# Optimization experiments

Measured on AMD Instinct MI355X. Metric: run time of the kernel, lower is better.

## Reference

```python
import jax, jax.numpy as jnp
import numpy as np

N_ATOMS = 5000
N_PAIRS = 160000
N_STRUCT = 16
N_SPECIES = 4
L_MAX = 2
K = 128            # k_max per l (rectangular)
N_BASIS = 8        # radial basis size
RAD_HIDDEN = 32    # radial MLP hidden
CUTOFF = 5.0
MSG_SCALE = 0.1767767   # ~1/sqrt(avg_degree)
INIT_SCALE = 0.2        # hypers['initial_scaling']


def _orthogonal(key, n):
    m = jax.random.normal(key, (n, n))
    q, r = jnp.linalg.qr(m)
    return q * jnp.sign(jnp.diag(r))[None, :]


def setup_inputs() -> dict:
    key = jax.random.key(0)
    ks = jax.random.split(key, 24)
    positions = jax.random.normal(ks[0], (N_ATOMS, 3)) * 1.5
    cells = jax.random.normal(ks[1], (N_STRUCT, 3, 3)) * 0.5
    species = jax.random.randint(ks[2], (N_ATOMS,), 0, N_SPECIES)
    cell_shifts = jax.random.randint(ks[3], (N_PAIRS, 3), 0, 3).astype(jnp.int32)
    center_indices = jax.random.randint(ks[4], (N_PAIRS,), 0, N_ATOMS)
    neighbor_indices = jax.random.randint(ks[5], (N_PAIRS,), 0, N_ATOMS)
    structure_pairs = jax.random.randint(ks[6], (N_PAIRS,), 0, N_STRUCT)
    s = lambda k, sh, f: jax.random.normal(k, sh) * f
    params = dict(
        embed=s(ks[7], (N_SPECIES, K), 1.0),
        rad_w1=s(ks[8], (N_BASIS, RAD_HIDDEN), 0.3), rad_b1=jnp.zeros((RAD_HIDDEN,)),
        rad_w2=s(ks[9], (RAD_HIDDEN, (L_MAX + 1) * K), 0.3), rad_b2=jnp.zeros(((L_MAX + 1) * K,)),
        erad_w1=s(ks[10], (N_BASIS, RAD_HIDDEN), 0.3), erad_b1=jnp.zeros((RAD_HIDDEN,)),
        erad_w2=s(ks[11], (RAD_HIDDEN, (L_MAX + 1) * K), 0.3), erad_b2=jnp.zeros(((L_MAX + 1) * K,)),
        mix_a=s(ks[12], (L_MAX + 1, K), 0.5),
        emix_a=s(ks[13], (L_MAX + 1, K), 0.5),
        head_w1=s(ks[14], (K, K), 0.1), head_b1=jnp.zeros((K,)),
        head_w2=s(ks[15], (K, K), 0.1), head_b2=jnp.zeros((K,)),
        last_w=s(ks[16], (K, 1), 0.1), last_b=jnp.zeros((1,)),
        U2=_orthogonal(ks[20], 9),  # orthogonal CG change-of-basis, U @ U.T = I
    )
    return dict(positions=positions, cells=cells, species=species,
                cell_shifts=cell_shifts, center_indices=center_indices,
                neighbor_indices=neighbor_indices, structure_pairs=structure_pairs,
                **params)


def _sph(unit):
    # real spherical harmonics up to l=2, inputs are unit vectors [P,3]
    x, y, z = unit[:, 0], unit[:, 1], unit[:, 2]
    sh0 = jnp.ones_like(x)[:, None]
    sh1 = jnp.stack([y, z, x], axis=1)
    c = jnp.sqrt(3.0)
    sh2 = jnp.stack([c * x * y, c * y * z, 0.5 * (3 * z * z - 1.0),
                     c * x * z, 0.5 * c * (x * x - y * y)], axis=1)
    return [sh0, sh1, sh2]


def _radial(d, w1, b1, w2, b2):
    # Gaussian radial basis * smooth cutoff -> MLP -> per-l K channels
    centers = jnp.linspace(0.0, CUTOFF, N_BASIS)
    rb = jnp.exp(-((d[:, None] - centers[None, :]) ** 2) / (2.0 * 0.5 ** 2))
    fcut = jnp.where(d < CUTOFF, 0.5 * (jnp.cos(jnp.pi * d / CUTOFF) + 1.0), 0.0)
    h = jax.nn.silu((rb * fcut[:, None]) @ w1 + b1)
    return (h @ w2 + b2).reshape(-1, L_MAX + 1, K)  # [P, l, K]


def _uncouple(f, l, U2):
    # coupled [N, 2l+1, K] -> uncoupled matrix [N, 3, 3, K] (padded_l = 2)
    if l == 0:
        return f[:, :, None, :]
    n, _, k = f.shape
    vec = jnp.zeros((n, 9, k), f.dtype)
    off = 1 if l == 1 else 4
    vec = vec.at[:, off:off + 2 * l + 1, :].set(f)
    unc = jnp.einsum('qp,nqk->npk', U2, vec)  # U2.T @ vec
    return unc.reshape(n, 3, 3, k)


def _couple(unc, l, U2):
    if l == 0:
        return unc[:, :, 0, :]
    n, k = unc.shape[0], unc.shape[-1]
    vec = jnp.einsum('pq,nqk->npk', U2, unc.reshape(n, 9, k))
    off = 1 if l == 1 else 4
    return vec[:, off:off + 2 * l + 1, :]


def _cg_iterate(feats, U2, mix):
    # CG tensor product iteration in the uncoupled (matrix) basis:
    # matrix product A@A is equivariant under A -> D A D^T
    out = []
    for l, f in enumerate(feats):
        A = _uncouple(f, l, U2)
        C = jnp.einsum('nimk,nmjk->nijk', A, A)
        out.append(_couple(A + C * mix[l][None, None, None, :], l, U2))
    return out


def _forward(positions, cells, embed, rad_w1, rad_b1, rad_w2, rad_b2,
             erad_w1, erad_b1, erad_w2, erad_b2, mix_a, emix_a,
             head_w1, head_b1, head_w2, head_b2, last_w, last_b, U2,
             species, cell_shifts, center_indices, neighbor_indices, structure_pairs):
    # pair vectors with PBC shifts
    shifts = cell_shifts.astype(positions.dtype) - 1.0  # -> {-1,0,1}
    vec = positions[neighbor_indices] - positions[center_indices] \
        + jnp.einsum('pi,pij->pj', shifts, cells[structure_pairs])
    d = jnp.sqrt(jnp.sum(vec * vec, axis=1) + 1e-12)
    unit = vec / d[:, None]
    sh = [s * INIT_SCALE for s in _sph(unit)]
    Rk = _radial(d, rad_w1, rad_b1, rad_w2, rad_b2)      # [P, 3, K]
    emb_n = embed[species][neighbor_indices]             # [P, K]

    # invariant message passing: sh_l x radial x neighbor embedding, scatter to centers
    feats = []
    for l in range(L_MAX + 1):
        msg = sh[l][:, :, None] * Rk[:, l, None, :] * emb_n[:, None, :]
        feats.append(jax.ops.segment_sum(msg, center_indices, num_segments=N_ATOMS) * MSG_SCALE)

    feats = _cg_iterate(feats, U2, mix_a)

    # equivariant message passing layer
    Rke = _radial(d, erad_w1, erad_b1, erad_w2, erad_b2)
    inv_n = feats[0][neighbor_indices, 0, :]             # [P, K] invariant part
    new = []
    for l in range(L_MAX + 1):
        g = feats[l][neighbor_indices]                   # [P, 2l+1, K]
        msg = sh[l][:, :, None] * Rke[:, l, None, :] * inv_n[:, None, :] \
            + Rke[:, 0, None, :] * g
        new.append(feats[l] + jax.ops.segment_sum(msg, center_indices, num_segments=N_ATOMS) * MSG_SCALE)

    feats = _cg_iterate(new, U2, emix_a)

    # scalar (l=0) MLP head + last linear layer
    h = feats[0][:, 0, :]
    h = jax.nn.silu(h @ head_w1 + head_b1)
    h = jax.nn.silu(h @ head_w2 + head_b2)
    return h @ last_w + last_b  # [N_ATOMS, 1]


def reference(positions, cells, species, cell_shifts, center_indices,
              neighbor_indices, structure_pairs, embed, rad_w1, rad_b1, rad_w2,
              rad_b2, erad_w1, erad_b1, erad_w2, erad_b2, mix_a, emix_a,
              head_w1, head_b1, head_w2, head_b2, last_w, last_b, U2):
    return _forward(positions, cells, embed, rad_w1, rad_b1, rad_w2, rad_b2,
                    erad_w1, erad_b1, erad_w2, erad_b2, mix_a, emix_a,
                    head_w1, head_b1, head_w2, head_b2, last_w, last_b, U2,
                    species, cell_shifts, center_indices, neighbor_indices,
                    structure_pairs)
```

## Files before the change

### kernel.cpp

```cpp
#include <hip/hip_runtime.h>

constexpr int   kAtoms  = 5000;
constexpr int   kPairs  = 160000;
constexpr int   KD      = 128;
constexpr int   NB      = 8;
constexpr int   RH      = 32;
constexpr float kCutoff = 5.0f;
constexpr float kPi     = 3.14159265358979323846f;
constexpr float C1 = 0.2f * 0.1767767f;
constexpr float C2 = 1.2f * 0.1767767f;
constexpr int   CHUNK = 32;

__device__ __forceinline__ float silu(float x) { return x / (1.0f + __expf(-x)); }


__global__ __launch_bounds__(256) void hist_kernel(
    const int* __restrict__ ctr, int* __restrict__ cnt)
{
    int p = blockIdx.x * 256 + threadIdx.x;
    atomicAdd(cnt + ctr[p], 1);
}

__global__ __launch_bounds__(1024) void scan_kernel(
    const int* __restrict__ cnt, int* __restrict__ off, int* __restrict__ cur)
{
    __shared__ int s_part[1024];
    const int CH = 5;
    int t = threadIdx.x;
    int base = t * CH;
    int loc[CH];
    int run = 0;
    #pragma unroll
    for (int i = 0; i < CH; i++) {
        int idx = base + i;
        int v = (idx < kAtoms) ? cnt[idx] : 0;
        loc[i] = run;
        run += v;
    }
    s_part[t] = run;
    __syncthreads();
    for (int st = 1; st < 1024; st <<= 1) {
        int v = (t >= st) ? s_part[t - st] : 0;
        __syncthreads();
        s_part[t] += v;
        __syncthreads();
    }
    int excl = (t > 0) ? s_part[t - 1] : 0;
    #pragma unroll
    for (int i = 0; i < CH; i++) {
        int idx = base + i;
        if (idx < kAtoms) { off[idx] = excl + loc[i]; cur[idx] = excl + loc[i]; }
    }
    if (t == 1023) off[kAtoms] = s_part[1023];
}

__global__ __launch_bounds__(256) void build_kernel(
    const float* __restrict__ pos, const float* __restrict__ cells,
    const int* __restrict__ species, const int* __restrict__ shifts,
    const int* __restrict__ ctr, const int* __restrict__ nbr,
    const int* __restrict__ spair,
    int* __restrict__ cur, int* __restrict__ nbrs_s, int* __restrict__ specs_s,
    float* __restrict__ rbf_s)
{
    int p = blockIdx.x * 256 + threadIdx.x;
    int ci = ctr[p], ni = nbr[p], sp = spair[p];
    float s0 = (float)shifts[p * 3 + 0] - 1.0f;
    float s1 = (float)shifts[p * 3 + 1] - 1.0f;
    float s2 = (float)shifts[p * 3 + 2] - 1.0f;
    const float* C = cells + sp * 9;
    float vx = pos[ni * 3 + 0] - pos[ci * 3 + 0] + s0 * C[0] + s1 * C[3] + s2 * C[6];
    float vy = pos[ni * 3 + 1] - pos[ci * 3 + 1] + s0 * C[1] + s1 * C[4] + s2 * C[7];
    float vz = pos[ni * 3 + 2] - pos[ci * 3 + 2] + s0 * C[2] + s1 * C[5] + s2 * C[8];
    float d = sqrtf(vx * vx + vy * vy + vz * vz + 1e-12f);
    float fcut = (d < kCutoff) ? 0.5f * (__cosf(kPi * d / kCutoff) + 1.0f) : 0.0f;

    int slot = atomicAdd(cur + ci, 1);
    nbrs_s[slot]  = ni;
    specs_s[slot] = species[ni];

    float r[NB];
    #pragma unroll
    for (int i = 0; i < NB; i++) {
        float tt = d - (kCutoff / (NB - 1)) * (float)i;
        r[i] = __expf(-2.0f * tt * tt) * fcut;
    }
    float4* dst = (float4*)(rbf_s + (size_t)slot * NB);
    dst[0] = make_float4(r[0], r[1], r[2], r[3]);
    dst[1] = make_float4(r[4], r[5], r[6], r[7]);
}

__global__ __launch_bounds__(128) void f0_kernel(
    const float* __restrict__ rbf_s, const int* __restrict__ specs_s,
    const int* __restrict__ off,
    const float* __restrict__ embed,
    const float* __restrict__ w1, const float* __restrict__ b1,
    const float* __restrict__ w2, const float* __restrict__ b2,
    const float* __restrict__ mix,
    float* __restrict__ G0)
{
    __shared__ float s_w1[NB][RH];
    __shared__ float s_b1v[RH];
    __shared__ float s_Hp[2][2][4][RH];
    __shared__ float s_H[2][4][RH];
    __shared__ float s_np[2][2][4];
    __shared__ float s_nc[2][4];

    int t = threadIdx.x;
    int w = t >> 6;
    int t64 = t & 63;
    for (int idx = t; idx < NB * RH; idx += 128)
        s_w1[idx >> 5][idx & 31] = w1[idx];
    if (t < RH) s_b1v[t] = b1[t];
    __syncthreads();

    int a = blockIdx.x * 2 + w;
    int start = off[a], m = off[a + 1] - start;

    int g = t64 >> 5, j = t64 & 31;
    float H0 = 0, H1 = 0, H2 = 0, H3 = 0;
    int   n0 = 0, n1 = 0, n2 = 0, n3 = 0;
    float b1j = s_b1v[j];
    for (int pr = g; pr < m; pr += 2) {
        const float* rb = rbf_s + (size_t)(start + pr) * NB;
        float acc = b1j;
        #pragma unroll
        for (int i = 0; i < NB; i++) acc += rb[i] * s_w1[i][j];
        float h = silu(acc);
        int s = specs_s[start + pr];
        H0 += (s == 0) ? h : 0.0f;  H1 += (s == 1) ? h : 0.0f;
        H2 += (s == 2) ? h : 0.0f;  H3 += (s == 3) ? h : 0.0f;
        n0 += (s == 0); n1 += (s == 1); n2 += (s == 2); n3 += (s == 3);
    }
    s_Hp[w][g][0][j] = H0; s_Hp[w][g][1][j] = H1;
    s_Hp[w][g][2][j] = H2; s_Hp[w][g][3][j] = H3;
    if (j == 0) {
        s_np[w][g][0] = (float)n0; s_np[w][g][1] = (float)n1;
        s_np[w][g][2] = (float)n2; s_np[w][g][3] = (float)n3;
    }
    __syncthreads();
    for (int e = t64; e < 4 * RH; e += 64) {
        int s = e >> 5, jj = e & 31;
        s_H[w][s][jj] = s_Hp[w][0][s][jj] + s_Hp[w][1][s][jj];
    }
    if (t64 < 4) s_nc[w][t64] = s_np[w][0][t64] + s_np[w][1][t64];
    __syncthreads();

    float nc0 = s_nc[w][0], nc1 = s_nc[w][1], nc2 = s_nc[w][2], nc3 = s_nc[w][3];
    #pragma unroll
    for (int half = 0; half < 2; half++) {
        int k = t64 + 64 * half;
        float e0 = embed[0 * KD + k], e1 = embed[1 * KD + k];
        float e2 = embed[2 * KD + k], e3 = embed[3 * KD + k];
        float P0 = 0, P1 = 0, P2 = 0, P3 = 0;
        #pragma unroll 2
        for (int jq = 0; jq < RH / 4; jq++) {
            float4 h0 = *(const float4*)&s_H[w][0][4 * jq];
            float4 h1 = *(const float4*)&s_H[w][1][4 * jq];
            float4 h2 = *(const float4*)&s_H[w][2][4 * jq];
            float4 h3 = *(const float4*)&s_H[w][3][4 * jq];
            float wa = w2[(4 * jq + 0) * (3 * KD) + k];
            float wb = w2[(4 * jq + 1) * (3 * KD) + k];
            float wc = w2[(4 * jq + 2) * (3 * KD) + k];
            float wd = w2[(4 * jq + 3) * (3 * KD) + k];
            P0 += h0.x * wa + h0.y * wb + h0.z * wc + h0.w * wd;
            P1 += h1.x * wa + h1.y * wb + h1.z * wc + h1.w * wd;
            P2 += h2.x * wa + h2.y * wb + h2.z * wc + h2.w * wd;
            P3 += h3.x * wa + h3.y * wb + h3.z * wc + h3.w * wd;
        }
        float F = b2[k] * (nc0 * e0 + nc1 * e1 + nc2 * e2 + nc3 * e3)
                + e0 * P0 + e1 * P1 + e2 * P2 + e3 * P3;
        float F0v = C1 * F;
        G0[(size_t)a * KD + k] = F0v + F0v * F0v * mix[k];
    }
}

__global__ __launch_bounds__(64, 2) void d0_kernel(
    const float* __restrict__ rbf_s, const int* __restrict__ nbrs_s,
    const int* __restrict__ off,
    const float* __restrict__ w1, const float* __restrict__ b1,
    const float* __restrict__ w2, const float* __restrict__ b2,
    const float* __restrict__ emix,
    const float* __restrict__ G0,
    float* __restrict__ V)
{
    __shared__ float s_w1[NB][RH];
    __shared__ float s_b1v[RH];
    __shared__ float s_h[CHUNK][RH];
    __shared__ int   s_nbr[CHUNK];

    int t = threadIdx.x;
    for (int idx = t; idx < NB * RH; idx += 64)
        s_w1[idx >> 5][idx & 31] = w1[idx];
    if (t < RH) s_b1v[t] = b1[t];
    __syncthreads();

    int a = blockIdx.x;
    int start = off[a], end = off[a + 1];
    int k0 = t, k1 = t + 64;

    float w2c0[RH], w2c1[RH];
    #pragma unroll
    for (int j = 0; j < RH; j++) {
        w2c0[j] = w2[j * (3 * KD) + k0];
        w2c1[j] = w2[j * (3 * KD) + k1];
    }
    float b2k0 = b2[k0], b2k1 = b2[k1];

    int g = t >> 5, j = t & 31;
    float b1j = s_b1v[j];

    float Dacc0 = 0.0f, Dacc1 = 0.0f;
    for (int c = start; c < end; c += CHUNK) {
        int m = min(CHUNK, end - c);
        __syncthreads();
        for (int pr = g; pr < m; pr += 2) {
            const float* rb = rbf_s + (size_t)(c + pr) * NB;
            float acc = b1j;
            #pragma unroll
            for (int i = 0; i < NB; i++) acc += rb[i] * s_w1[i][j];
            s_h[pr][j] = silu(acc);
        }
        if (t < m) s_nbr[t] = nbrs_s[c + t];
        __syncthreads();

        const float* gb = G0 + (size_t)s_nbr[0] * KD;
        float gv0_next = gb[k0];
        float gv1_next = gb[k1];
        for (int i = 0; i < m; i++) {
            float gv0 = gv0_next, gv1 = gv1_next;
            if (i + 1 < m) {
                const float* gn = G0 + (size_t)s_nbr[i + 1] * KD;
                gv0_next = gn[k0];
                gv1_next = gn[k1];
            }
            float R0 = b2k0, R1 = b2k1;
            #pragma unroll
            for (int jq = 0; jq < RH / 4; jq++) {
                float4 h4 = *(const float4*)&s_h[i][4 * jq];
                R0 += h4.x * w2c0[4 * jq + 0] + h4.y * w2c0[4 * jq + 1]
                    + h4.z * w2c0[4 * jq + 2] + h4.w * w2c0[4 * jq + 3];
                R1 += h4.x * w2c1[4 * jq + 0] + h4.y * w2c1[4 * jq + 1]
                    + h4.z * w2c1[4 * jq + 2] + h4.w * w2c1[4 * jq + 3];
            }
            Dacc0 += R0 * gv0;
            Dacc1 += R1 * gv1;
        }
    }
    float n0 = G0[(size_t)a * KD + k0] + C2 * Dacc0;
    float n1 = G0[(size_t)a * KD + k1] + C2 * Dacc1;
    V[(size_t)a * KD + k0] = n0 + n0 * n0 * emix[k0];
    V[(size_t)a * KD + k1] = n1 + n1 * n1 * emix[k1];
}

__global__ __launch_bounds__(128) void head_kernel(
    const float* __restrict__ V,
    const float* __restrict__ w1, const float* __restrict__ b1,
    const float* __restrict__ w2, const float* __restrict__ b2,
    const float* __restrict__ lw, const float* __restrict__ lb,
    float* __restrict__ out)
{
    __shared__ float s_a[8][KD];
    __shared__ float s_b[8][KD];
    int j = threadIdx.x;
    int abase = blockIdx.x * 8;

    #pragma unroll
    for (int a = 0; a < 8; a++) {
        int ga = abase + a;
        s_a[a][j] = (ga < kAtoms) ? V[(size_t)ga * KD + j] : 0.0f;
    }
    __syncthreads();

    float acc[8];
    float bj = b1[j];
    #pragma unroll
    for (int a = 0; a < 8; a++) acc[a] = bj;
    for (int kk = 0; kk < KD; kk += 4) {
        float wa = w1[(kk + 0) * KD + j], wb = w1[(kk + 1) * KD + j];
        float wc = w1[(kk + 2) * KD + j], wd = w1[(kk + 3) * KD + j];
        #pragma unroll
        for (int a = 0; a < 8; a++) {
            float4 v = *(const float4*)&s_a[a][kk];
            acc[a] += v.x * wa + v.y * wb + v.z * wc + v.w * wd;
        }
    }
    #pragma unroll
    for (int a = 0; a < 8; a++) s_b[a][j] = silu(acc[a]);
    __syncthreads();

    float b2j = b2[j];
    #pragma unroll
    for (int a = 0; a < 8; a++) acc[a] = b2j;
    for (int kk = 0; kk < KD; kk += 4) {
        float wa = w2[(kk + 0) * KD + j], wb = w2[(kk + 1) * KD + j];
        float wc = w2[(kk + 2) * KD + j], wd = w2[(kk + 3) * KD + j];
        #pragma unroll
        for (int a = 0; a < 8; a++) {
            float4 v = *(const float4*)&s_b[a][kk];
            acc[a] += v.x * wa + v.y * wb + v.z * wc + v.w * wd;
        }
    }
    float lwj = lw[j];
    __syncthreads();
    #pragma unroll
    for (int a = 0; a < 8; a++) s_a[a][j] = silu(acc[a]) * lwj;
    __syncthreads();
    for (int s = 64; s > 0; s >>= 1) {
        if (j < s) {
            #pragma unroll
            for (int a = 0; a < 8; a++) s_a[a][j] += s_a[a][j + s];
        }
        __syncthreads();
    }
    if (j < 8) {
        int ga = abase + j;
        if (ga < kAtoms) out[ga] = s_a[j][0] + lb[0];
    }
}

extern "C" void kernel_launch(void* const* d_in, const int* in_sizes, int n_in,
                              void* d_out, int out_size, void* d_ws, size_t ws_size,
                              hipStream_t stream) {
    const float* positions = (const float*)d_in[0];
    const float* cells     = (const float*)d_in[1];
    const int*   species   = (const int*)d_in[2];
    const int*   shifts    = (const int*)d_in[3];
    const int*   ctr       = (const int*)d_in[4];
    const int*   nbr       = (const int*)d_in[5];
    const int*   spair     = (const int*)d_in[6];
    const float* embed     = (const float*)d_in[7];
    const float* rad_w1    = (const float*)d_in[8];
    const float* rad_b1    = (const float*)d_in[9];
    const float* rad_w2    = (const float*)d_in[10];
    const float* rad_b2    = (const float*)d_in[11];
    const float* erad_w1   = (const float*)d_in[12];
    const float* erad_b1   = (const float*)d_in[13];
    const float* erad_w2   = (const float*)d_in[14];
    const float* erad_b2   = (const float*)d_in[15];
    const float* mix_a     = (const float*)d_in[16];
    const float* emix_a    = (const float*)d_in[17];
    const float* head_w1   = (const float*)d_in[18];
    const float* head_b1   = (const float*)d_in[19];
    const float* head_w2   = (const float*)d_in[20];
    const float* head_b2   = (const float*)d_in[21];
    const float* last_w    = (const float*)d_in[22];
    const float* last_b    = (const float*)d_in[23];

    float* rbf_s = (float*)d_ws;
    float* G0    = rbf_s + (size_t)kPairs * NB;
    float* V     = G0    + (size_t)kAtoms * KD;
    int*   cnt   = (int*)(V + (size_t)kAtoms * KD);
    int*   off   = cnt + kAtoms;
    int*   cur   = off + kAtoms + 1;
    int*   nbrs  = cur + kAtoms;
    int*   specs = nbrs + kPairs;

    hipMemsetAsync(cnt, 0, kAtoms * sizeof(int), stream);

    hist_kernel<<<kPairs / 256, 256, 0, stream>>>(ctr, cnt);
    scan_kernel<<<1, 1024, 0, stream>>>(cnt, off, cur);
    build_kernel<<<kPairs / 256, 256, 0, stream>>>(
        positions, cells, species, shifts, ctr, nbr, spair,
        cur, nbrs, specs, rbf_s);

    f0_kernel<<<kAtoms / 2, 128, 0, stream>>>(
        rbf_s, specs, off, embed, rad_w1, rad_b1, rad_w2, rad_b2,
        mix_a, G0);

    d0_kernel<<<kAtoms, 64, 0, stream>>>(
        rbf_s, nbrs, off, erad_w1, erad_b1, erad_w2, erad_b2,
        emix_a, G0, V);

    head_kernel<<<(kAtoms + 7) / 8, 128, 0, stream>>>(
        V, head_w1, head_b1, head_w2, head_b2, last_w, last_b,
        (float*)d_out);
}
```

Before: 223.7 us.

## Fuse histogram into scan kernel and pack four atoms per block

Merges the memset, the global-atomic histogram and the scan into one single-block kernel that counts with shared-memory atomics. f0 and d0 now process four atoms per 256-thread block, with d0 looping to the block-wide maximum chunk count so that its syncthreads stay uniform. The rbf loads become float4, and the G0 gather in d0 is prefetched four neighbours ahead. The fused prep kernel runs on a single workgroup that reads all 160k indices, which could serialize. The wider d0 blocks may also hold more registers and waste lanes on atoms with fewer neighbours.

```diff
diff --git a/kernel.cpp b/kernel.cpp
--- a/kernel.cpp
+++ b/kernel.cpp
@@ -10,30 +10,30 @@
 constexpr float C1 = 0.2f * 0.1767767f;
 constexpr float C2 = 1.2f * 0.1767767f;
 constexpr int   CHUNK = 32;
+constexpr int   AT    = 4;
 
 __device__ __forceinline__ float silu(float x) { return x / (1.0f + __expf(-x)); }
 
 
-__global__ __launch_bounds__(256) void hist_kernel(
-    const int* __restrict__ ctr, int* __restrict__ cnt)
+__global__ __launch_bounds__(1024) void prep_kernel(
+    const int* __restrict__ ctr, int* __restrict__ off, int* __restrict__ cur)
 {
-    int p = blockIdx.x * 256 + threadIdx.x;
-    atomicAdd(cnt + ctr[p], 1);
-}
-
-__global__ __launch_bounds__(1024) void scan_kernel(
-    const int* __restrict__ cnt, int* __restrict__ off, int* __restrict__ cur)
-{
+    __shared__ int s_cnt[kAtoms];
     __shared__ int s_part[1024];
+    int t = threadIdx.x;
+    for (int i = t; i < kAtoms; i += 1024) s_cnt[i] = 0;
+    __syncthreads();
+    for (int p = t; p < kPairs; p += 1024) atomicAdd(&s_cnt[ctr[p]], 1);
+    __syncthreads();
+
     const int CH = 5;
-    int t = threadIdx.x;
     int base = t * CH;
     int loc[CH];
     int run = 0;
     #pragma unroll
     for (int i = 0; i < CH; i++) {
         int idx = base + i;
-        int v = (idx < kAtoms) ? cnt[idx] : 0;
+        int v = (idx < kAtoms) ? s_cnt[idx] : 0;
         loc[i] = run;
         run += v;
     }
@@ -89,7 +89,7 @@
     dst[1] = make_float4(r[4], r[5], r[6], r[7]);
 }
 
-__global__ __launch_bounds__(128) void f0_kernel(
+__global__ __launch_bounds__(256) void f0_kernel(
     const float* __restrict__ rbf_s, const int* __restrict__ specs_s,
     const int* __restrict__ off,
     const float* __restrict__ embed,
@@ -100,20 +100,20 @@
 {
     __shared__ float s_w1[NB][RH];
     __shared__ float s_b1v[RH];
-    __shared__ float s_Hp[2][2][4][RH];
-    __shared__ float s_H[2][4][RH];
-    __shared__ float s_np[2][2][4];
-    __shared__ float s_nc[2][4];
+    __shared__ float s_Hp[AT][2][4][RH];
+    __shared__ float s_H[AT][4][RH];
+    __shared__ float s_np[AT][2][4];
+    __shared__ float s_nc[AT][4];
 
     int t = threadIdx.x;
     int w = t >> 6;
     int t64 = t & 63;
-    for (int idx = t; idx < NB * RH; idx += 128)
+    for (int idx = t; idx < NB * RH; idx += 256)
         s_w1[idx >> 5][idx & 31] = w1[idx];
     if (t < RH) s_b1v[t] = b1[t];
     __syncthreads();
 
-    int a = blockIdx.x * 2 + w;
+    int a = blockIdx.x * AT + w;
     int start = off[a], m = off[a + 1] - start;
 
     int g = t64 >> 5, j = t64 & 31;
@@ -121,10 +121,13 @@
     int   n0 = 0, n1 = 0, n2 = 0, n3 = 0;
     float b1j = s_b1v[j];
     for (int pr = g; pr < m; pr += 2) {
-        const float* rb = rbf_s + (size_t)(start + pr) * NB;
-        float acc = b1j;
-        #pragma unroll
-        for (int i = 0; i < NB; i++) acc += rb[i] * s_w1[i][j];
+        const float4* rb4 = (const float4*)(rbf_s + (size_t)(start + pr) * NB);
+        float4 ra = rb4[0], rb = rb4[1];
+        float acc = b1j
+            + ra.x * s_w1[0][j] + ra.y * s_w1[1][j]
+            + ra.z * s_w1[2][j] + ra.w * s_w1[3][j]
+            + rb.x * s_w1[4][j] + rb.y * s_w1[5][j]
+            + rb.z * s_w1[6][j] + rb.w * s_w1[7][j];
         float h = silu(acc);
         int s = specs_s[start + pr];
         H0 += (s == 0) ? h : 0.0f;  H1 += (s == 1) ? h : 0.0f;
@@ -174,7 +177,7 @@
     }
 }
 
-__global__ __launch_bounds__(64, 2) void d0_kernel(
+__global__ __launch_bounds__(256, 2) void d0_kernel(
     const float* __restrict__ rbf_s, const int* __restrict__ nbrs_s,
     const int* __restrict__ off,
     const float* __restrict__ w1, const float* __restrict__ b1,
@@ -185,19 +188,30 @@
 {
     __shared__ float s_w1[NB][RH];
     __shared__ float s_b1v[RH];
-    __shared__ float s_h[CHUNK][RH];
-    __shared__ int   s_nbr[CHUNK];
+    __shared__ float s_h[AT][CHUNK][RH];
+    __shared__ int   s_nbr[AT][CHUNK];
 
     int t = threadIdx.x;
-    for (int idx = t; idx < NB * RH; idx += 64)
+    for (int idx = t; idx < NB * RH; idx += 256)
         s_w1[idx >> 5][idx & 31] = w1[idx];
     if (t < RH) s_b1v[t] = b1[t];
-    __syncthreads();
-
-    int a = blockIdx.x;
+
+    int w    = t >> 6;
+    int lane = t & 63;
+    int abase = blockIdx.x * AT;
+    int a = abase + w;
+
     int start = off[a], end = off[a + 1];
-    int k0 = t, k1 = t + 64;
-
+
+    int nch_max = 0;
+    #pragma unroll
+    for (int u = 0; u < AT; u++) {
+        int s_ = off[abase + u], e_ = off[abase + u + 1];
+        int nc = (e_ - s_ + CHUNK - 1) / CHUNK;
+        nch_max = max(nch_max, nc);
+    }
+
+    int k0 = lane, k1 = lane + 64;
     float w2c0[RH], w2c1[RH];
     #pragma unroll
     for (int j = 0; j < RH; j++) {
@@ -206,44 +220,67 @@
     }
     float b2k0 = b2[k0], b2k1 = b2[k1];
 
-    int g = t >> 5, j = t & 31;
+    int g2 = lane >> 5, j = lane & 31;
+    __syncthreads();
     float b1j = s_b1v[j];
 
     float Dacc0 = 0.0f, Dacc1 = 0.0f;
-    for (int c = start; c < end; c += CHUNK) {
+    for (int ch = 0; ch < nch_max; ch++) {
+        int c = start + ch * CHUNK;
         int m = min(CHUNK, end - c);
+        if (m > 0) {
+            for (int pr = g2; pr < m; pr += 2) {
+                const float4* rb4 = (const float4*)(rbf_s + (size_t)(c + pr) * NB);
+                float4 ra = rb4[0], rb = rb4[1];
+                float acc = b1j
+                    + ra.x * s_w1[0][j] + ra.y * s_w1[1][j]
+                    + ra.z * s_w1[2][j] + ra.w * s_w1[3][j]
+                    + rb.x * s_w1[4][j] + rb.y * s_w1[5][j]
+                    + rb.z * s_w1[6][j] + rb.w * s_w1[7][j];
+                s_h[w][pr][j] = silu(acc);
+            }
+            if (lane < m) s_nbr[w][lane] = nbrs_s[c + lane];
+        }
         __syncthreads();
-        for (int pr = g; pr < m; pr += 2) {
-            const float* rb = rbf_s + (size_t)(c + pr) * NB;
-            float acc = b1j;
+        if (m > 0) {
+            float ga0[4], ga1[4];
             #pragma unroll
-            for (int i = 0; i < NB; i++) acc += rb[i] * s_w1[i][j];
-            s_h[pr][j] = silu(acc);
-        }
-        if (t < m) s_nbr[t] = nbrs_s[c + t];
-        __syncthreads();
-
-        const float* gb = G0 + (size_t)s_nbr[0] * KD;
-        float gv0_next = gb[k0];
-        float gv1_next = gb[k1];
-        for (int i = 0; i < m; i++) {
-            float gv0 = gv0_next, gv1 = gv1_next;
-            if (i + 1 < m) {
-                const float* gn = G0 + (size_t)s_nbr[i + 1] * KD;
-                gv0_next = gn[k0];
-                gv1_next = gn[k1];
+            for (int u = 0; u < 4; u++) {
+                if (u < m) {
+                    const float* gp = G0 + (size_t)s_nbr[w][u] * KD;
+                    ga0[u] = gp[k0]; ga1[u] = gp[k1];
+                }
             }
-            float R0 = b2k0, R1 = b2k1;
-            #pragma unroll
-            for (int jq = 0; jq < RH / 4; jq++) {
-                float4 h4 = *(const float4*)&s_h[i][4 * jq];
-                R0 += h4.x * w2c0[4 * jq + 0] + h4.y * w2c0[4 * jq + 1]
-                    + h4.z * w2c0[4 * jq + 2] + h4.w * w2c0[4 * jq + 3];
-                R1 += h4.x * w2c1[4 * jq + 0] + h4.y * w2c1[4 * jq + 1]
-                    + h4.z * w2c1[4 * jq + 2] + h4.w * w2c1[4 * jq + 3];
+            for (int ib = 0; ib < m; ib += 4) {
+                float gb0[4], gb1[4];
+                #pragma unroll
+                for (int u = 0; u < 4; u++) { gb0[u] = ga0[u]; gb1[u] = ga1[u]; }
+                #pragma unroll
+                for (int u = 0; u < 4; u++) {
+                    int ii = ib + 4 + u;
+                    if (ii < m) {
+                        const float* gp = G0 + (size_t)s_nbr[w][ii] * KD;
+                        ga0[u] = gp[k0]; ga1[u] = gp[k1];
+                    }
+                }
+                #pragma unroll
+                for (int u = 0; u < 4; u++) {
+                    int i = ib + u;
+                    if (i < m) {
+                        float R0 = b2k0, R1 = b2k1;
+                        #pragma unroll
+                        for (int jq = 0; jq < RH / 4; jq++) {
+                            float4 h4 = *(const float4*)&s_h[w][i][4 * jq];
+                            R0 += h4.x * w2c0[4 * jq + 0] + h4.y * w2c0[4 * jq + 1]
+                                + h4.z * w2c0[4 * jq + 2] + h4.w * w2c0[4 * jq + 3];
+                            R1 += h4.x * w2c1[4 * jq + 0] + h4.y * w2c1[4 * jq + 1]
+                                + h4.z * w2c1[4 * jq + 2] + h4.w * w2c1[4 * jq + 3];
+                        }
+                        Dacc0 += R0 * gb0[u];
+                        Dacc1 += R1 * gb1[u];
+                    }
+                }
             }
-            Dacc0 += R0 * gv0;
-            Dacc1 += R1 * gv1;
         }
     }
     float n0 = G0[(size_t)a * KD + k0] + C2 * Dacc0;
@@ -355,19 +392,17 @@
     int*   nbrs  = cur + kAtoms;
     int*   specs = nbrs + kPairs;
 
-    hipMemsetAsync(cnt, 0, kAtoms * sizeof(int), stream);
-
-    hist_kernel<<<kPairs / 256, 256, 0, stream>>>(ctr, cnt);
-    scan_kernel<<<1, 1024, 0, stream>>>(cnt, off, cur);
+    prep_kernel<<<1, 1024, 0, stream>>>(ctr, off, cur);
+
     build_kernel<<<kPairs / 256, 256, 0, stream>>>(
         positions, cells, species, shifts, ctr, nbr, spair,
         cur, nbrs, specs, rbf_s);
 
-    f0_kernel<<<kAtoms / 2, 128, 0, stream>>>(
+    f0_kernel<<<kAtoms / AT, 256, 0, stream>>>(
         rbf_s, specs, off, embed, rad_w1, rad_b1, rad_w2, rad_b2,
         mix_a, G0);
 
-    d0_kernel<<<kAtoms, 64, 0, stream>>>(
+    d0_kernel<<<kAtoms / AT, 256, 0, stream>>>(
         rbf_s, nbrs, off, erad_w1, erad_b1, erad_w2, erad_b2,
         emix_a, G0, V);
 
```

Result: slower. 254.3 us (+13.7%).
